# Performance work log

Measured on AMD Instinct MI355X. Metric: run time of the kernel, lower is better.

## Reference

```python
import jax, jax.numpy as jnp
import numpy as np

N_NODES = 50000
N_EDGES = 400000
IN_FEATS = 16
HIDDEN = 32
EDGE_FEATS = 16
EDGE_MLP_HID = 8 * IN_FEATS  # 128
N_CLS_EDGES = 100000
OUT_FEATS = 2


def setup_inputs() -> dict:
    key = jax.random.key(0)
    ks = jax.random.split(key, 12)
    s = 0.05
    return {
        "node_feats": jax.random.normal(ks[0], (N_NODES, IN_FEATS), jnp.float32),
        "edge_feats": jax.random.normal(ks[1], (N_EDGES, EDGE_FEATS), jnp.float32),
        "src": jax.random.randint(ks[2], (N_EDGES,), 0, N_NODES),
        "dst": jax.random.randint(ks[3], (N_EDGES,), 0, N_NODES),
        "edge_indices": jax.random.randint(ks[4], (N_CLS_EDGES,), 0, N_EDGES),
        "en_w1": s * jax.random.normal(ks[5], (EDGE_FEATS, EDGE_MLP_HID), jnp.float32),
        "en_b1": jnp.zeros((EDGE_MLP_HID,), jnp.float32),
        "en_w2": s * jax.random.normal(ks[6], (EDGE_MLP_HID, HIDDEN * IN_FEATS), jnp.float32),
        "en_b2": jnp.zeros((HIDDEN * IN_FEATS,), jnp.float32),
        "conv_b": jnp.zeros((HIDDEN,), jnp.float32),
        "cls_w1": s * jax.random.normal(ks[7], (2 * HIDDEN + EDGE_FEATS, HIDDEN), jnp.float32),
        "cls_b1": jnp.zeros((HIDDEN,), jnp.float32),
        "cls_w2": s * jax.random.normal(ks[8], (HIDDEN, OUT_FEATS), jnp.float32),
        "cls_b2": jnp.zeros((OUT_FEATS,), jnp.float32),
    }


def reference(node_feats, edge_feats, src, dst, edge_indices,
              en_w1, en_b1, en_w2, en_b2, conv_b,
              cls_w1, cls_b1, cls_w2, cls_b2):
    # edge MLP -> per-edge weight matrices [E, in_feats, hidden]
    ew = jax.nn.relu(edge_feats @ en_w1 + en_b1) @ en_w2 + en_b2
    W = ew.reshape(-1, IN_FEATS, HIDDEN)
    # gather src features, per-edge matvec, mean-scatter to dst (DGL NNConv, aggregator='mean')
    msg = jnp.einsum('ei,eih->eh', node_feats[src], W)  # [E, hidden]
    agg = jax.ops.segment_sum(msg, dst, num_segments=N_NODES)
    deg = jax.ops.segment_sum(jnp.ones((N_EDGES,), msg.dtype), dst, num_segments=N_NODES)
    h = jax.nn.relu(agg / jnp.maximum(deg, 1.0)[:, None] + conv_b)  # dropout is identity at eval
    # edge classifier on selected edges
    s_idx = src[edge_indices]
    d_idx = dst[edge_indices]
    edge_input = jnp.concatenate([h[s_idx], h[d_idx], edge_feats[edge_indices]], axis=1)
    logits = jax.nn.relu(edge_input @ cls_w1 + cls_b1) @ cls_w2 + cls_b2
    return logits
```

## Files before the change

kernel.cpp:

```cpp
#include <hip/hip_runtime.h>
#include <stdint.h>

#define N_NODES   50000
#define N_EDGES   400000
#define IN_FEATS  16
#define HIDDEN    32
#define K1        128
#define NOUT      512
#define N_CLS     100000
#define CAP       40
#define TILE_E    128
#define FUSED_BLOCKS (N_EDGES / TILE_E)

typedef float  f32x4  __attribute__((ext_vector_type(4)));
typedef __bf16 bf16x8 __attribute__((ext_vector_type(8)));

__device__ __forceinline__ unsigned short f32_bf16(float f) {
    union { float f; uint32_t u; } c; c.f = f;
    uint32_t r = c.u + 0x7fffu + ((c.u >> 16) & 1u);
    return (unsigned short)(r >> 16);
}

__device__ __forceinline__ void gload_lds16(const unsigned short* g, unsigned short* l) {
    __builtin_amdgcn_global_load_lds(
        (const __attribute__((address_space(1))) unsigned int*)(g),
        (__attribute__((address_space(3))) unsigned int*)(l),
        16, 0, 0);
}

__global__ void prep_and_slots(const float* __restrict__ w2, const float* __restrict__ w1,
                               const int* __restrict__ dst,
                               unsigned short* __restrict__ w2ts, unsigned short* __restrict__ w1t,
                               int* __restrict__ cursor, int* __restrict__ slots) {
    int gid = blockIdx.x * 256 + threadIdx.x;
    if (gid < NOUT * K1) {
        int n = gid >> 7, k = gid & 127;
        w2ts[n * 128 + (k ^ ((n & 15) << 3))] = f32_bf16(w2[k * 512 + n]);
    } else if (gid < NOUT * K1 + 4096) {
        int t = gid - NOUT * K1;
        int n = t >> 5, k = t & 31;
        w1t[n * 32 + k] = (k < 16) ? f32_bf16(w1[k * 128 + n]) : (unsigned short)0;
    }
    if (gid < N_EDGES) {
        int d = dst[gid];
        int pos = atomicAdd(&cursor[d], 1);
        if (pos < CAP) slots[d * CAP + pos] = gid;
    }
}

__global__ __launch_bounds__(256, 4) void fused_msg(
    const float* __restrict__ nf, const float* __restrict__ ef,
    const int* __restrict__ src,
    const unsigned short* __restrict__ w1t, const float* __restrict__ b1,
    const unsigned short* __restrict__ w2ts, const float* __restrict__ b2,
    float* __restrict__ msg)
{
    __shared__ __align__(16) unsigned short sAmem[128 * 128];

    const int tid  = threadIdx.x;
    const int lane = tid & 63;
    const int w    = tid >> 6;
    const int l15  = lane & 15;
    const int lg   = lane >> 4;
    const int key  = (l15 & 7) << 3;
    const int key2 = l15 << 3;
    const int e0   = blockIdx.x * TILE_E;

    unsigned short* buf0 = sAmem;
    unsigned short* buf1 = sAmem + 8192;

    auto stage = [&](int cc, unsigned short* buf) {
        #pragma unroll
        for (int i = 0; i < 4; ++i)
            gload_lds16(&w2ts[cc * 8192 + (w * 4 + i) * 512 + lane * 8],
                        &buf[(w * 4 + i) * 512]);
    };

    const int ea = e0 + w * 32 + l15;
    const int eb = ea + 16;
    const int sa0 = src[ea];
    const int sa1 = src[eb];

    {
        bf16x8 w1f0 = *reinterpret_cast<const bf16x8*>(&w1t[((2 * w) * 16 + l15) * 32 + lg * 8]);
        bf16x8 w1f1 = *reinterpret_cast<const bf16x8*>(&w1t[((2 * w + 1) * 16 + l15) * 32 + lg * 8]);
        float4 q0 = *reinterpret_cast<const float4*>(&b1[(2 * w) * 16 + lg * 4]);
        float4 q1 = *reinterpret_cast<const float4*>(&b1[(2 * w + 1) * 16 + lg * 4]);
        #pragma unroll
        for (int et = 0; et < 8; ++et) {
            int e = e0 + et * 16 + l15;
            bf16x8 aef;
            if (lg < 2) {
                float4 f0 = *reinterpret_cast<const float4*>(&ef[e * 16 + lg * 8]);
                float4 f1 = *reinterpret_cast<const float4*>(&ef[e * 16 + lg * 8 + 4]);
                unsigned short t8[8] = { f32_bf16(f0.x), f32_bf16(f0.y), f32_bf16(f0.z), f32_bf16(f0.w),
                                         f32_bf16(f1.x), f32_bf16(f1.y), f32_bf16(f1.z), f32_bf16(f1.w) };
                aef = *reinterpret_cast<const bf16x8*>(t8);
            } else {
                aef = bf16x8(0);
            }
            int le = et * 16 + l15;
            f32x4 c0 = { q0.x, q0.y, q0.z, q0.w };
            c0 = __builtin_amdgcn_mfma_f32_16x16x32_bf16(w1f0, aef, c0, 0, 0, 0);
            uint32_t u0 = (uint32_t)f32_bf16(fmaxf(c0[0], 0.f)) | ((uint32_t)f32_bf16(fmaxf(c0[1], 0.f)) << 16);
            uint32_t u1 = (uint32_t)f32_bf16(fmaxf(c0[2], 0.f)) | ((uint32_t)f32_bf16(fmaxf(c0[3], 0.f)) << 16);
            uint2 pk0 = { u0, u1 };
            *reinterpret_cast<uint2*>(&sAmem[le * 128 + (((2 * w) * 16 + lg * 4) ^ key)]) = pk0;

            f32x4 c1 = { q1.x, q1.y, q1.z, q1.w };
            c1 = __builtin_amdgcn_mfma_f32_16x16x32_bf16(w1f1, aef, c1, 0, 0, 0);
            uint32_t u2 = (uint32_t)f32_bf16(fmaxf(c1[0], 0.f)) | ((uint32_t)f32_bf16(fmaxf(c1[1], 0.f)) << 16);
            uint32_t u3 = (uint32_t)f32_bf16(fmaxf(c1[2], 0.f)) | ((uint32_t)f32_bf16(fmaxf(c1[3], 0.f)) << 16);
            uint2 pk1 = { u2, u3 };
            *reinterpret_cast<uint2*>(&sAmem[le * 128 + (((2 * w + 1) * 16 + lg * 4) ^ key)]) = pk1;
        }
    }
    __syncthreads();

    bf16x8 aF[2][4];
    #pragma unroll
    for (int et = 0; et < 2; ++et) {
        int le = w * 32 + et * 16 + l15;
        #pragma unroll
        for (int kb = 0; kb < 4; ++kb)
            aF[et][kb] = *reinterpret_cast<const bf16x8*>(
                &sAmem[le * 128 + ((kb * 32 + lg * 8) ^ key)]);
    }
    __syncthreads();

    stage(0, buf0);
    stage(1, buf1);
    __syncthreads();

    float msgv[2][8];
    #pragma unroll
    for (int et = 0; et < 2; ++et)
        #pragma unroll
        for (int q = 0; q < 8; ++q) msgv[et][q] = 0.f;

    #pragma unroll 1
    for (int c = 0; c < 8; ++c) {
        const unsigned short* sCur = (c & 1) ? buf1 : buf0;

        float2 xw0 = *reinterpret_cast<const float2*>(&nf[sa0 * 16 + c * 2]);
        float2 xw1 = *reinterpret_cast<const float2*>(&nf[sa1 * 16 + c * 2]);

        #pragma unroll
        for (int f = 0; f < 4; ++f) {
            int n = f * 16 + l15;
            bf16x8 bw[4];
            #pragma unroll
            for (int kb = 0; kb < 4; ++kb)
                bw[kb] = *reinterpret_cast<const bf16x8*>(
                    &sCur[n * 128 + ((kb * 32 + lg * 8) ^ key2)]);
            float4 b2q = *reinterpret_cast<const float4*>(&b2[c * 64 + f * 16 + lg * 4]);
            f32x4 a0 = { b2q.x, b2q.y, b2q.z, b2q.w };
            f32x4 a1 = a0;
            #pragma unroll
            for (int kb = 0; kb < 4; ++kb) {
                a0 = __builtin_amdgcn_mfma_f32_16x16x32_bf16(bw[kb], aF[0][kb], a0, 0, 0, 0);
                a1 = __builtin_amdgcn_mfma_f32_16x16x32_bf16(bw[kb], aF[1][kb], a1, 0, 0, 0);
            }
            const float x0 = (f >> 1) ? xw0.y : xw0.x;
            const float x1 = (f >> 1) ? xw1.y : xw1.x;
            const int s = (f & 1) * 4;
            #pragma unroll
            for (int r = 0; r < 4; ++r) {
                msgv[0][s + r] += x0 * a0[r];
                msgv[1][s + r] += x1 * a1[r];
            }
        }

        if (c < 7) {
            __syncthreads();
            if (c + 2 < 8) stage(c + 2, (c & 1) ? buf1 : buf0);
        }
    }

    #pragma unroll
    for (int et = 0; et < 2; ++et) {
        int e = et ? eb : ea;
        #pragma unroll
        for (int half = 0; half < 2; ++half) {
            float4 o = { msgv[et][half * 4 + 0], msgv[et][half * 4 + 1],
                         msgv[et][half * 4 + 2], msgv[et][half * 4 + 3] };
            *reinterpret_cast<float4*>(&msg[e * 32 + half * 16 + lg * 4]) = o;
        }
    }
}

__global__ __launch_bounds__(256) void aggregate_h(
    const float* __restrict__ msg, const int* __restrict__ cursor,
    const int* __restrict__ slots, const float* __restrict__ conv_b,
    float* __restrict__ h)
{
    int t = blockIdx.x * 256 + threadIdx.x;
    int n = t >> 3;
    if (n >= N_NODES) return;
    int q = t & 7;
    int d = cursor[n];
    int dm = d < CAP ? d : CAP;
    const int* row = &slots[n * CAP];
    float4 s = { 0.f, 0.f, 0.f, 0.f };
    int j = 0;
    for (; j + 2 <= dm; j += 2) {
        int ee0 = row[j], ee1 = row[j + 1];
        float4 v0 = *reinterpret_cast<const float4*>(&msg[ee0 * 32 + q * 4]);
        float4 v1 = *reinterpret_cast<const float4*>(&msg[ee1 * 32 + q * 4]);
        s.x += v0.x + v1.x; s.y += v0.y + v1.y; s.z += v0.z + v1.z; s.w += v0.w + v1.w;
    }
    if (j < dm) {
        float4 v = *reinterpret_cast<const float4*>(&msg[row[j] * 32 + q * 4]);
        s.x += v.x; s.y += v.y; s.z += v.z; s.w += v.w;
    }
    float inv = 1.0f / fmaxf((float)d, 1.f);
    float4 cb = *reinterpret_cast<const float4*>(&conv_b[q * 4]);
    float4 o;
    o.x = fmaxf(s.x * inv + cb.x, 0.f);
    o.y = fmaxf(s.y * inv + cb.y, 0.f);
    o.z = fmaxf(s.z * inv + cb.z, 0.f);
    o.w = fmaxf(s.w * inv + cb.w, 0.f);
    *reinterpret_cast<float4*>(&h[n * 32 + q * 4]) = o;
}

__global__ __launch_bounds__(256) void classifier(
    const float* __restrict__ h, const float* __restrict__ ef,
    const int* __restrict__ src, const int* __restrict__ dst, const int* __restrict__ eidx,
    const float* __restrict__ w1, const float* __restrict__ b1,
    const float* __restrict__ w2, const float* __restrict__ b2, float* __restrict__ out)
{
    __shared__ float sIn[32][84];
    __shared__ float sW1[80 * 32];
    __shared__ float sHid[32][36];
    __shared__ int   sE[32 * 3];
    int tid = threadIdx.x;
    int eb  = blockIdx.x * 32;

    for (int i = tid; i < 640; i += 256)
        *reinterpret_cast<float4*>(&sW1[i * 4]) = *reinterpret_cast<const float4*>(&w1[i * 4]);
    if (tid < 32) {
        int ei = eidx[eb + tid];
        sE[tid * 3 + 0] = ei;
        sE[tid * 3 + 1] = src[ei];
        sE[tid * 3 + 2] = dst[ei];
    }
    __syncthreads();
    {
        int e = tid >> 3, l8 = tid & 7;
        int ei = sE[e * 3 + 0], sn = sE[e * 3 + 1], dn = sE[e * 3 + 2];
        #pragma unroll
        for (int j = 0; j < 10; ++j) {
            int c = l8 + j * 8;
            float v;
            if (c < 32)      v = h[sn * 32 + c];
            else if (c < 64) v = h[dn * 32 + (c - 32)];
            else             v = ef[ei * 16 + (c - 64)];
            sIn[e][c] = v;
        }
    }
    __syncthreads();
    {
        int e = tid >> 3, j0 = (tid & 7) * 4;
        float4 acc = *reinterpret_cast<const float4*>(&b1[j0]);
        #pragma unroll 8
        for (int k = 0; k < 80; ++k) {
            float x = sIn[e][k];
            float4 wv = *reinterpret_cast<const float4*>(&sW1[k * 32 + j0]);
            acc.x += x * wv.x; acc.y += x * wv.y; acc.z += x * wv.z; acc.w += x * wv.w;
        }
        sHid[e][j0 + 0] = fmaxf(acc.x, 0.f);
        sHid[e][j0 + 1] = fmaxf(acc.y, 0.f);
        sHid[e][j0 + 2] = fmaxf(acc.z, 0.f);
        sHid[e][j0 + 3] = fmaxf(acc.w, 0.f);
    }
    __syncthreads();
    if (tid < 64) {
        int e = tid >> 1, o = tid & 1;
        float acc = b2[o];
        #pragma unroll
        for (int j = 0; j < 32; ++j) acc += sHid[e][j] * w2[j * 2 + o];
        out[(eb + e) * 2 + o] = acc;
    }
}

extern "C" void kernel_launch(void* const* d_in, const int* in_sizes, int n_in,
                              void* d_out, int out_size, void* d_ws, size_t ws_size,
                              hipStream_t stream) {
    const float* nf     = (const float*)d_in[0];
    const float* ef     = (const float*)d_in[1];
    const int*   src    = (const int*)d_in[2];
    const int*   dst    = (const int*)d_in[3];
    const int*   eidx   = (const int*)d_in[4];
    const float* en_w1  = (const float*)d_in[5];
    const float* en_b1  = (const float*)d_in[6];
    const float* en_w2  = (const float*)d_in[7];
    const float* en_b2  = (const float*)d_in[8];
    const float* conv_b = (const float*)d_in[9];
    const float* cls_w1 = (const float*)d_in[10];
    const float* cls_b1 = (const float*)d_in[11];
    const float* cls_w2 = (const float*)d_in[12];
    const float* cls_b2 = (const float*)d_in[13];
    float* out = (float*)d_out;

    char* ws = (char*)d_ws;
    unsigned short* w2ts   = (unsigned short*)(ws);
    unsigned short* w1t    = (unsigned short*)(ws + 131072);
    int*            cursor = (int*)(ws + 139264);
    int*            slots  = (int*)(ws + 339264);
    float*          msgb   = (float*)(ws + 8339264);
    float*          h      = (float*)(ws + 59539264);

    hipMemsetAsync(cursor, 0, N_NODES * sizeof(int), stream);
    prep_and_slots<<<(N_EDGES + 255) / 256, 256, 0, stream>>>(en_w2, en_w1, dst, w2ts, w1t, cursor, slots);
    fused_msg<<<FUSED_BLOCKS, 256, 0, stream>>>(nf, ef, src, w1t, en_b1, w2ts, en_b2, msgb);
    aggregate_h<<<(N_NODES * 8 + 255) / 256, 256, 0, stream>>>(msgb, cursor, slots, conv_b, h);
    classifier<<<N_CLS / 32, 256, 0, stream>>>(h, ef, src, dst, eidx, cls_w1, cls_b1, cls_w2, cls_b2, out);
}
```

Before: 140.3 us.

## Use two-wave blocks with four edge tiles per wave and store messages in bf16

The fused message kernel drops from 256 to 128 threads per block. Each wave now handles 64 edges, so every B fragment loaded from LDS feeds four MFMAs instead of two, and each wave stages twice as many weight segments. The per-edge message buffer is written as bf16 instead of fp32, which halves the traffic written by fused_msg and read by the gather in aggregate_h. The cost is more registers per thread, fewer waves per block (occupancy hint changed to 2), and added rounding error in the messages before they are averaged.

```diff
diff --git a/kernel.cpp b/kernel.cpp
--- a/kernel.cpp
+++ b/kernel.cpp
@@ -20,6 +20,8 @@
     uint32_t r = c.u + 0x7fffu + ((c.u >> 16) & 1u);
     return (unsigned short)(r >> 16);
 }
+__device__ __forceinline__ float bf_lo(uint32_t u) { union { uint32_t x; float f; } c; c.x = u << 16;          return c.f; }
+__device__ __forceinline__ float bf_hi(uint32_t u) { union { uint32_t x; float f; } c; c.x = u & 0xFFFF0000u;  return c.f; }
 
 __device__ __forceinline__ void gload_lds16(const unsigned short* g, unsigned short* l) {
     __builtin_amdgcn_global_load_lds(
@@ -48,12 +50,12 @@
     }
 }
 
-__global__ __launch_bounds__(256, 4) void fused_msg(
+__global__ __launch_bounds__(128, 2) void fused_msg(
     const float* __restrict__ nf, const float* __restrict__ ef,
     const int* __restrict__ src,
     const unsigned short* __restrict__ w1t, const float* __restrict__ b1,
     const unsigned short* __restrict__ w2ts, const float* __restrict__ b2,
-    float* __restrict__ msg)
+    unsigned short* __restrict__ msg)
 {
     __shared__ __align__(16) unsigned short sAmem[128 * 128];
 
@@ -71,21 +73,25 @@
 
     auto stage = [&](int cc, unsigned short* buf) {
         #pragma unroll
-        for (int i = 0; i < 4; ++i)
-            gload_lds16(&w2ts[cc * 8192 + (w * 4 + i) * 512 + lane * 8],
-                        &buf[(w * 4 + i) * 512]);
+        for (int i = 0; i < 8; ++i) {
+            int seg = w * 8 + i;
+            gload_lds16(&w2ts[cc * 8192 + seg * 512 + lane * 8], &buf[seg * 512]);
+        }
     };
 
-    const int ea = e0 + w * 32 + l15;
-    const int eb = ea + 16;
-    const int sa0 = src[ea];
-    const int sa1 = src[eb];
+    int sa[4];
+    #pragma unroll
+    for (int et = 0; et < 4; ++et) sa[et] = src[e0 + w * 64 + et * 16 + l15];
 
     {
-        bf16x8 w1f0 = *reinterpret_cast<const bf16x8*>(&w1t[((2 * w) * 16 + l15) * 32 + lg * 8]);
-        bf16x8 w1f1 = *reinterpret_cast<const bf16x8*>(&w1t[((2 * w + 1) * 16 + l15) * 32 + lg * 8]);
-        float4 q0 = *reinterpret_cast<const float4*>(&b1[(2 * w) * 16 + lg * 4]);
-        float4 q1 = *reinterpret_cast<const float4*>(&b1[(2 * w + 1) * 16 + lg * 4]);
+        bf16x8 w1f[4];
+        float4 b1q[4];
+        #pragma unroll
+        for (int t = 0; t < 4; ++t) {
+            int n1b = w * 64 + t * 16;
+            w1f[t] = *reinterpret_cast<const bf16x8*>(&w1t[(n1b + l15) * 32 + lg * 8]);
+            b1q[t] = *reinterpret_cast<const float4*>(&b1[n1b + lg * 4]);
+        }
         #pragma unroll
         for (int et = 0; et < 8; ++et) {
             int e = e0 + et * 16 + l15;
@@ -100,27 +106,23 @@
                 aef = bf16x8(0);
             }
             int le = et * 16 + l15;
-            f32x4 c0 = { q0.x, q0.y, q0.z, q0.w };
-            c0 = __builtin_amdgcn_mfma_f32_16x16x32_bf16(w1f0, aef, c0, 0, 0, 0);
-            uint32_t u0 = (uint32_t)f32_bf16(fmaxf(c0[0], 0.f)) | ((uint32_t)f32_bf16(fmaxf(c0[1], 0.f)) << 16);
-            uint32_t u1 = (uint32_t)f32_bf16(fmaxf(c0[2], 0.f)) | ((uint32_t)f32_bf16(fmaxf(c0[3], 0.f)) << 16);
-            uint2 pk0 = { u0, u1 };
-            *reinterpret_cast<uint2*>(&sAmem[le * 128 + (((2 * w) * 16 + lg * 4) ^ key)]) = pk0;
-
-            f32x4 c1 = { q1.x, q1.y, q1.z, q1.w };
-            c1 = __builtin_amdgcn_mfma_f32_16x16x32_bf16(w1f1, aef, c1, 0, 0, 0);
-            uint32_t u2 = (uint32_t)f32_bf16(fmaxf(c1[0], 0.f)) | ((uint32_t)f32_bf16(fmaxf(c1[1], 0.f)) << 16);
-            uint32_t u3 = (uint32_t)f32_bf16(fmaxf(c1[2], 0.f)) | ((uint32_t)f32_bf16(fmaxf(c1[3], 0.f)) << 16);
-            uint2 pk1 = { u2, u3 };
-            *reinterpret_cast<uint2*>(&sAmem[le * 128 + (((2 * w + 1) * 16 + lg * 4) ^ key)]) = pk1;
-        }
-    }
-    __syncthreads();
-
-    bf16x8 aF[2][4];
+            #pragma unroll
+            for (int t = 0; t < 4; ++t) {
+                f32x4 c = { b1q[t].x, b1q[t].y, b1q[t].z, b1q[t].w };
+                c = __builtin_amdgcn_mfma_f32_16x16x32_bf16(w1f[t], aef, c, 0, 0, 0);
+                uint32_t u0 = (uint32_t)f32_bf16(fmaxf(c[0], 0.f)) | ((uint32_t)f32_bf16(fmaxf(c[1], 0.f)) << 16);
+                uint32_t u1 = (uint32_t)f32_bf16(fmaxf(c[2], 0.f)) | ((uint32_t)f32_bf16(fmaxf(c[3], 0.f)) << 16);
+                uint2 pk = { u0, u1 };
+                *reinterpret_cast<uint2*>(&sAmem[le * 128 + ((w * 64 + t * 16 + lg * 4) ^ key)]) = pk;
+            }
+        }
+    }
+    __syncthreads();
+
+    bf16x8 aF[4][4];
     #pragma unroll
-    for (int et = 0; et < 2; ++et) {
-        int le = w * 32 + et * 16 + l15;
+    for (int et = 0; et < 4; ++et) {
+        int le = w * 64 + et * 16 + l15;
         #pragma unroll
         for (int kb = 0; kb < 4; ++kb)
             aF[et][kb] = *reinterpret_cast<const bf16x8*>(
@@ -132,9 +134,9 @@
     stage(1, buf1);
     __syncthreads();
 
-    float msgv[2][8];
+    float msgv[4][8];
     #pragma unroll
-    for (int et = 0; et < 2; ++et)
+    for (int et = 0; et < 4; ++et)
         #pragma unroll
         for (int q = 0; q < 8; ++q) msgv[et][q] = 0.f;
 
@@ -142,8 +144,10 @@
     for (int c = 0; c < 8; ++c) {
         const unsigned short* sCur = (c & 1) ? buf1 : buf0;
 
-        float2 xw0 = *reinterpret_cast<const float2*>(&nf[sa0 * 16 + c * 2]);
-        float2 xw1 = *reinterpret_cast<const float2*>(&nf[sa1 * 16 + c * 2]);
+        float2 xw[4];
+        #pragma unroll
+        for (int et = 0; et < 4; ++et)
+            xw[et] = *reinterpret_cast<const float2*>(&nf[sa[et] * 16 + c * 2]);
 
         #pragma unroll
         for (int f = 0; f < 4; ++f) {
@@ -155,19 +159,22 @@
                     &sCur[n * 128 + ((kb * 32 + lg * 8) ^ key2)]);
             float4 b2q = *reinterpret_cast<const float4*>(&b2[c * 64 + f * 16 + lg * 4]);
             f32x4 a0 = { b2q.x, b2q.y, b2q.z, b2q.w };
-            f32x4 a1 = a0;
+            f32x4 a1 = a0, a2 = a0, a3 = a0;
             #pragma unroll
             for (int kb = 0; kb < 4; ++kb) {
                 a0 = __builtin_amdgcn_mfma_f32_16x16x32_bf16(bw[kb], aF[0][kb], a0, 0, 0, 0);
                 a1 = __builtin_amdgcn_mfma_f32_16x16x32_bf16(bw[kb], aF[1][kb], a1, 0, 0, 0);
+                a2 = __builtin_amdgcn_mfma_f32_16x16x32_bf16(bw[kb], aF[2][kb], a2, 0, 0, 0);
+                a3 = __builtin_amdgcn_mfma_f32_16x16x32_bf16(bw[kb], aF[3][kb], a3, 0, 0, 0);
             }
-            const float x0 = (f >> 1) ? xw0.y : xw0.x;
-            const float x1 = (f >> 1) ? xw1.y : xw1.x;
             const int s = (f & 1) * 4;
+            const int xs = f >> 1;
             #pragma unroll
             for (int r = 0; r < 4; ++r) {
-                msgv[0][s + r] += x0 * a0[r];
-                msgv[1][s + r] += x1 * a1[r];
+                msgv[0][s + r] += (xs ? xw[0].y : xw[0].x) * a0[r];
+                msgv[1][s + r] += (xs ? xw[1].y : xw[1].x) * a1[r];
+                msgv[2][s + r] += (xs ? xw[2].y : xw[2].x) * a2[r];
+                msgv[3][s + r] += (xs ? xw[3].y : xw[3].x) * a3[r];
             }
         }
 
@@ -178,19 +185,22 @@
     }
 
     #pragma unroll
-    for (int et = 0; et < 2; ++et) {
-        int e = et ? eb : ea;
+    for (int et = 0; et < 4; ++et) {
+        int e = e0 + w * 64 + et * 16 + l15;
         #pragma unroll
         for (int half = 0; half < 2; ++half) {
-            float4 o = { msgv[et][half * 4 + 0], msgv[et][half * 4 + 1],
-                         msgv[et][half * 4 + 2], msgv[et][half * 4 + 3] };
-            *reinterpret_cast<float4*>(&msg[e * 32 + half * 16 + lg * 4]) = o;
+            uint32_t p0 = (uint32_t)f32_bf16(msgv[et][half * 4 + 0])
+                        | ((uint32_t)f32_bf16(msgv[et][half * 4 + 1]) << 16);
+            uint32_t p1 = (uint32_t)f32_bf16(msgv[et][half * 4 + 2])
+                        | ((uint32_t)f32_bf16(msgv[et][half * 4 + 3]) << 16);
+            uint2 o = { p0, p1 };
+            *reinterpret_cast<uint2*>(&msg[e * 32 + half * 16 + lg * 4]) = o;
         }
     }
 }
 
 __global__ __launch_bounds__(256) void aggregate_h(
-    const float* __restrict__ msg, const int* __restrict__ cursor,
+    const unsigned short* __restrict__ msg, const int* __restrict__ cursor,
     const int* __restrict__ slots, const float* __restrict__ conv_b,
     float* __restrict__ h)
 {
@@ -202,16 +212,9 @@
     int dm = d < CAP ? d : CAP;
     const int* row = &slots[n * CAP];
     float4 s = { 0.f, 0.f, 0.f, 0.f };
-    int j = 0;
-    for (; j + 2 <= dm; j += 2) {
-        int ee0 = row[j], ee1 = row[j + 1];
-        float4 v0 = *reinterpret_cast<const float4*>(&msg[ee0 * 32 + q * 4]);
-        float4 v1 = *reinterpret_cast<const float4*>(&msg[ee1 * 32 + q * 4]);
-        s.x += v0.x + v1.x; s.y += v0.y + v1.y; s.z += v0.z + v1.z; s.w += v0.w + v1.w;
-    }
-    if (j < dm) {
-        float4 v = *reinterpret_cast<const float4*>(&msg[row[j] * 32 + q * 4]);
-        s.x += v.x; s.y += v.y; s.z += v.z; s.w += v.w;
+    for (int j = 0; j < dm; ++j) {
+        uint2 u = *reinterpret_cast<const uint2*>(&msg[row[j] * 32 + q * 4]);
+        s.x += bf_lo(u.x); s.y += bf_hi(u.x); s.z += bf_lo(u.y); s.w += bf_hi(u.y);
     }
     float inv = 1.0f / fmaxf((float)d, 1.f);
     float4 cb = *reinterpret_cast<const float4*>(&conv_b[q * 4]);
@@ -307,12 +310,12 @@
     unsigned short* w1t    = (unsigned short*)(ws + 131072);
     int*            cursor = (int*)(ws + 139264);
     int*            slots  = (int*)(ws + 339264);
-    float*          msgb   = (float*)(ws + 8339264);
-    float*          h      = (float*)(ws + 59539264);
+    unsigned short* msgb   = (unsigned short*)(ws + 8339264);
+    float*          h      = (float*)(ws + 33939264);
 
     hipMemsetAsync(cursor, 0, N_NODES * sizeof(int), stream);
     prep_and_slots<<<(N_EDGES + 255) / 256, 256, 0, stream>>>(en_w2, en_w1, dst, w2ts, w1t, cursor, slots);
-    fused_msg<<<FUSED_BLOCKS, 256, 0, stream>>>(nf, ef, src, w1t, en_b1, w2ts, en_b2, msgb);
+    fused_msg<<<FUSED_BLOCKS, 128, 0, stream>>>(nf, ef, src, w1t, en_b1, w2ts, en_b2, msgb);
     aggregate_h<<<(N_NODES * 8 + 255) / 256, 256, 0, stream>>>(msgb, cursor, slots, conv_b, h);
     classifier<<<N_CLS / 32, 256, 0, stream>>>(h, ef, src, dst, eidx, cls_w1, cls_b1, cls_w2, cls_b2, out);
 }
```

Result: no change. 141.5 us (+0.8%).
